# Optimization experiments

Measured on AMD Instinct MI355X. Metric: run time of the kernel, lower is better.

## Reference

```python
import jax, jax.numpy as jnp
import numpy as np

EPS = 1e-8
LN_EPS = 1e-5

def _layernorm(x, g, b):
    mu = jnp.mean(x, axis=-1, keepdims=True)
    var = jnp.mean((x - mu) ** 2, axis=-1, keepdims=True)
    return (x - mu) / jnp.sqrt(var + LN_EPS) * g + b

def setup_inputs() -> dict:
    key = jax.random.key(0)
    ks = jax.random.split(key, 10)
    B, S = 8192, 4096
    input_dim, hidden_dim = 4, 256
    h4 = hidden_dim // 4  # 64
    price_series = jax.random.uniform(ks[0], (B, S, 1), dtype=jnp.float32) + 0.5
    # 4 parallel encoders stacked on leading axis: Linear(input_dim->h4) + LayerNorm(h4)
    enc_w = jax.random.normal(ks[1], (4, input_dim, h4), dtype=jnp.float32) * 0.5
    enc_b = jax.random.normal(ks[2], (4, h4), dtype=jnp.float32) * 0.02
    enc_g = jnp.ones((4, h4), dtype=jnp.float32)
    enc_beta = jnp.zeros((4, h4), dtype=jnp.float32)
    # regime head: Linear(hidden_dim->64) + ReLU + (Dropout eval=identity) + Linear(64->4)
    head_w1 = jax.random.normal(ks[3], (hidden_dim, 64), dtype=jnp.float32) * 0.0625
    head_b1 = jnp.zeros((64,), dtype=jnp.float32)
    head_w2 = jax.random.normal(ks[4], (64, 4), dtype=jnp.float32) * 0.125
    head_b2 = jnp.zeros((4,), dtype=jnp.float32)
    return {"price_series": price_series, "enc_w": enc_w, "enc_b": enc_b,
            "enc_g": enc_g, "enc_beta": enc_beta,
            "head_w1": head_w1, "head_b1": head_b1,
            "head_w2": head_w2, "head_b2": head_b2}

def reference(price_series, enc_w, enc_b, enc_g, enc_beta, head_w1, head_b1, head_w2, head_b2):
    prices = price_series[:, :, 0]  # [B, S]
    B, S = prices.shape
    # Rolling SMA(20) with clamped window start, via cumsum (single pass, no per-step loop)
    csum = jnp.concatenate([jnp.zeros((B, 1), prices.dtype), jnp.cumsum(prices, axis=1)], axis=1)  # [B, S+1]
    i = jnp.arange(S)
    start20 = jnp.maximum(0, i - 19)
    cnt20 = (i - start20 + 1).astype(prices.dtype)
    sma20 = (csum[:, i + 1] - csum[:, start20]) / cnt20  # [B, S]
    trend_signal = (prices - sma20) / (sma20 + EPS)
    f_trend = jnp.mean(trend_signal, axis=1, keepdims=True)  # [B,1]
    # momentum over last 10 steps
    p_last = prices[:, -1:]
    p_m10 = prices[:, -10:-9]
    f_mom = (p_last - p_m10) / (p_m10 + EPS)  # [B,1]
    # mean reversion
    p_mean = jnp.mean(prices, axis=1, keepdims=True)
    f_mr = (p_last - p_mean) / (p_mean + EPS)  # [B,1]
    # cycle: coefficient of variation (torch.std is unbiased, ddof=1)
    f_cyc = jnp.std(prices, axis=1, ddof=1, keepdims=True) / (p_mean + EPS)  # [B,1]
    combined = jnp.concatenate([f_trend, f_mom, f_mr, f_cyc], axis=1)  # [B, 4]
    # 4 parallel encoders: Linear -> ReLU -> LayerNorm
    pre = jnp.einsum('bi,eio->ebo', combined, enc_w) + enc_b[:, None, :]  # [4, B, 64]
    feats = _layernorm(jax.nn.relu(pre), enc_g[:, None, :], enc_beta[:, None, :])  # [4, B, 64]
    # concat order: trend, momentum, mean_rev, cycle along feature dim
    regime_features = jnp.transpose(feats, (1, 0, 2)).reshape(B, -1)  # [B, 256]
    h = jax.nn.relu(regime_features @ head_w1 + head_b1)
    regime_probs = jax.nn.softmax(h @ head_w2 + head_b2, axis=1)  # [B, 4]
    return (regime_features, regime_probs)
```

## Files before the change

kernel.cpp:

```cpp
#include <hip/hip_runtime.h>

#define EPS 1e-8f
#define LN_EPS 1e-5f
#define NROWS 8192
#define SLEN 4096
#define PROBS_OFF 2097152
#define RPB 16

typedef __attribute__((ext_vector_type(8))) short bf16x8;
typedef __attribute__((ext_vector_type(4))) float f32x4;

__device__ __forceinline__ short f2bf(float f) {
    unsigned u = __float_as_uint(f);
    unsigned r = (u + 0x7FFFu + ((u >> 16) & 1u)) >> 16;
    return (short)r;
}

__device__ __forceinline__ void g2l16(const float4* g, float4* l) {
    __builtin_amdgcn_global_load_lds(
        (const __attribute__((address_space(1))) unsigned int*)g,
        (__attribute__((address_space(3))) unsigned int*)l,
        16, 0, 0);
}

__device__ __forceinline__ int swz(int s) { return s ^ ((s >> 3) & 7); }

__global__ __launch_bounds__(256) void k_fused(
    const float* __restrict__ prices, float* __restrict__ out,
    const float* __restrict__ enc_w, const float* __restrict__ enc_b,
    const float* __restrict__ enc_g, const float* __restrict__ enc_bt,
    const float* __restrict__ w1, const float* __restrict__ b1,
    const float* __restrict__ w2, const float* __restrict__ b2)
{
    __shared__ float4 sbuf[3][1032];
    __shared__ float red[4][3];
    __shared__ __align__(16) float comb[RPB][4];
    __shared__ short rfb[RPB][264];
    __shared__ float hbuf[RPB][68];

    const int t = threadIdx.x;
    const int lane = t & 63, wv = t >> 6;
    const int r0 = blockIdx.x * RPB;

    auto stage = [&](int r, int bi) {
        const float4* R4 = (const float4*)prices + (size_t)(r0 + r) * 1024;
        #pragma unroll
        for (int k = 0; k < 4; ++k) {
            const int base = 8 + 256 * k + 64 * wv;
            const int g = swz(base + lane) - 8;
            g2l16(R4 + g, &sbuf[bi][base]);
        }
    };

    float pm10_l = 0.f, plast_l = 0.f;

    auto compute_row = [&](int bi) {
        float4 q0 = sbuf[bi][swz(4 * t + 3)];
        float4 q1 = sbuf[bi][swz(4 * t + 4)];
        float4 q2 = sbuf[bi][swz(4 * t + 5)];
        float4 q3 = sbuf[bi][swz(4 * t + 6)];
        float4 q4 = sbuf[bi][swz(4 * t + 7)];
        float4 s0 = sbuf[bi][swz(4 * t + 8)];
        float4 s1 = sbuf[bi][swz(4 * t + 9)];
        float4 s2 = sbuf[bi][swz(4 * t + 10)];
        float4 s3 = sbuf[bi][swz(4 * t + 11)];

        float xv[16] = { s0.x, s0.y, s0.z, s0.w, s1.x, s1.y, s1.z, s1.w,
                         s2.x, s2.y, s2.z, s2.w, s3.x, s3.y, s3.z, s3.w };
        float ov[16] = { q0.x, q0.y, q0.z, q0.w, q1.x, q1.y, q1.z, q1.w,
                         q2.x, q2.y, q2.z, q2.w, q3.x, q3.y, q3.z, q3.w };

        float W = q0.y + q0.z + q0.w
                + q1.x + q1.y + q1.z + q1.w
                + q2.x + q2.y + q2.z + q2.w
                + q3.x + q3.y + q3.z + q3.w
                + q4.x + q4.y + q4.z + q4.w;

        float sum = 0.0f, sq = 0.0f, ts = 0.0f;
        if (t >= 2) {
            #pragma unroll
            for (int j = 0; j < 16; ++j) {
                float x = xv[j];
                W += (j == 0) ? x : (x - ov[j]);
                sum += x;
                sq = fmaf(x, x, sq);
                float num = fmaf(x, 20.0f, -W);
                float den = W + (20.0f * EPS);
                ts += num * __builtin_amdgcn_rcpf(den);
            }
        } else {
            const float pf = (float)(16 * t);
            #pragma unroll
            for (int j = 0; j < 16; ++j) {
                float x = xv[j];
                W += (j == 0) ? x : (x - ov[j]);
                sum += x;
                sq = fmaf(x, x, sq);
                float c = fminf(pf + (float)(j + 1), 20.0f);
                float num = fmaf(x, c, -W);
                float den = fmaf(EPS, c, W);
                ts += num * __builtin_amdgcn_rcpf(den);
            }
        }
        if (t == 255) { pm10_l = s1.z; plast_l = s3.w; }

        #pragma unroll
        for (int off = 32; off > 0; off >>= 1) {
            sum += __shfl_xor(sum, off);
            sq  += __shfl_xor(sq,  off);
            ts  += __shfl_xor(ts,  off);
        }
        if (lane == 0) { red[wv][0] = sum; red[wv][1] = sq; red[wv][2] = ts; }
    };

    auto finish_row = [&](int r) {
        if (t == 255) {
            float S = red[0][0] + red[1][0] + red[2][0] + red[3][0];
            float Q = red[0][1] + red[1][1] + red[2][1] + red[3][1];
            float T = red[0][2] + red[1][2] + red[2][2] + red[3][2];
            float mean = S * (1.0f / 4096.0f);
            float var  = fmaxf((Q - 4096.0f * mean * mean) * (1.0f / 4095.0f), 0.0f);
            comb[r][0] = T * (1.0f / 4096.0f);
            comb[r][1] = (plast_l - pm10_l) / (pm10_l + EPS);
            comb[r][2] = (plast_l - mean) / (mean + EPS);
            comb[r][3] = sqrtf(var) / (mean + EPS);
        }
    };

    if (t < 8) {
        const float4 z4 = make_float4(0.f, 0.f, 0.f, 0.f);
        sbuf[0][t] = z4; sbuf[1][t] = z4; sbuf[2][t] = z4;
    }
    stage(0, 0);
    stage(1, 1);

    for (int r = 0; r < RPB - 2; ++r) {
        stage(r + 2, (r + 2) % 3);
        asm volatile("s_waitcnt vmcnt(8) lgkmcnt(0)\ns_barrier" ::: "memory");
        __builtin_amdgcn_sched_barrier(0);
        compute_row(r % 3);
        asm volatile("s_waitcnt lgkmcnt(0)\ns_barrier" ::: "memory");
        finish_row(r);
    }
    asm volatile("s_waitcnt vmcnt(4) lgkmcnt(0)\ns_barrier" ::: "memory");
    __builtin_amdgcn_sched_barrier(0);
    compute_row((RPB - 2) % 3);
    asm volatile("s_waitcnt lgkmcnt(0)\ns_barrier" ::: "memory");
    finish_row(RPB - 2);
    asm volatile("s_waitcnt vmcnt(0) lgkmcnt(0)\ns_barrier" ::: "memory");
    __builtin_amdgcn_sched_barrier(0);
    compute_row((RPB - 1) % 3);
    asm volatile("s_waitcnt lgkmcnt(0)\ns_barrier" ::: "memory");
    finish_row(RPB - 1);

    const int l15 = lane & 15, q = lane >> 4;
    const int wave = wv;

    bf16x8 bfrag[8];
    #pragma unroll
    for (int kt = 0; kt < 8; ++kt) {
        #pragma unroll
        for (int j = 0; j < 8; ++j) {
            int k = kt * 32 + q * 8 + j;
            bfrag[kt][j] = f2bf(w1[k * 64 + wave * 16 + l15]);
        }
    }
    const float ew0  = enc_w[wave * 256 + lane];
    const float ew1v = enc_w[wave * 256 + 64 + lane];
    const float ew2v = enc_w[wave * 256 + 128 + lane];
    const float ew3v = enc_w[wave * 256 + 192 + lane];
    const float ebv = enc_b[t], egv = enc_g[t], btv = enc_bt[t];

    __syncthreads();

    for (int r = 0; r < RPB; r += 2) {
        float4 cba = *(const float4*)comb[r];
        float4 cbb = *(const float4*)comb[r + 1];
        float va = fmaf(cba.x, ew0, fmaf(cba.y, ew1v, fmaf(cba.z, ew2v, fmaf(cba.w, ew3v, ebv))));
        float vb = fmaf(cbb.x, ew0, fmaf(cbb.y, ew1v, fmaf(cbb.z, ew2v, fmaf(cbb.w, ew3v, ebv))));
        va = fmaxf(va, 0.0f);
        vb = fmaxf(vb, 0.0f);
        float sma = va, smb = vb;
        #pragma unroll
        for (int off = 32; off > 0; off >>= 1) {
            sma += __shfl_xor(sma, off);
            smb += __shfl_xor(smb, off);
        }
        float mua = sma * (1.0f / 64.0f);
        float mub = smb * (1.0f / 64.0f);
        float da = va - mua, db = vb - mub;
        float vsa = da * da, vsb = db * db;
        #pragma unroll
        for (int off = 32; off > 0; off >>= 1) {
            vsa += __shfl_xor(vsa, off);
            vsb += __shfl_xor(vsb, off);
        }
        float ya = fmaf(da * rsqrtf(vsa * (1.0f / 64.0f) + LN_EPS), egv, btv);
        float yb = fmaf(db * rsqrtf(vsb * (1.0f / 64.0f) + LN_EPS), egv, btv);
        out[(size_t)(r0 + r) * 256 + t] = ya;
        out[(size_t)(r0 + r + 1) * 256 + t] = yb;
        rfb[r][t] = f2bf(ya);
        rfb[r + 1][t] = f2bf(yb);
    }
    __syncthreads();

    f32x4 acc0 = {0.f, 0.f, 0.f, 0.f};
    #pragma unroll
    for (int kt = 0; kt < 8; ++kt) {
        bf16x8 a0 = *(const bf16x8*)&rfb[l15][kt * 32 + q * 8];
        acc0 = __builtin_amdgcn_mfma_f32_16x16x32_bf16(a0, bfrag[kt], acc0, 0, 0, 0);
    }

    const int col = wave * 16 + l15;
    const float b1v = b1[col];
    #pragma unroll
    for (int rg = 0; rg < 4; ++rg)
        hbuf[q * 4 + rg][col] = fmaxf(acc0[rg] + b1v, 0.0f);
    __syncthreads();

    if (t < 4 * RPB) {
        int r = t >> 2, c = t & 3;
        float a0 = 0.f, a1 = 0.f, a2 = 0.f, a3 = 0.f;
        #pragma unroll
        for (int j = 0; j < 16; ++j) {
            a0 = fmaf(hbuf[r][j],      w2[j * 4 + c],        a0);
            a1 = fmaf(hbuf[r][16 + j], w2[(16 + j) * 4 + c], a1);
            a2 = fmaf(hbuf[r][32 + j], w2[(32 + j) * 4 + c], a2);
            a3 = fmaf(hbuf[r][48 + j], w2[(48 + j) * 4 + c], a3);
        }
        float lg = b2[c] + ((a0 + a1) + (a2 + a3));
        float mx = fmaxf(lg, __shfl_xor(lg, 1, 4));
        mx = fmaxf(mx, __shfl_xor(mx, 2, 4));
        float ex = __expf(lg - mx);
        float s2 = ex + __shfl_xor(ex, 1, 4);
        s2 += __shfl_xor(s2, 2, 4);
        out[PROBS_OFF + (size_t)(r0 + r) * 4 + c] = ex / s2;
    }
}

extern "C" void kernel_launch(void* const* d_in, const int* in_sizes, int n_in,
                              void* d_out, int out_size, void* d_ws, size_t ws_size,
                              hipStream_t stream) {
    const float* prices  = (const float*)d_in[0];
    const float* enc_w   = (const float*)d_in[1];
    const float* enc_b   = (const float*)d_in[2];
    const float* enc_g   = (const float*)d_in[3];
    const float* enc_bt  = (const float*)d_in[4];
    const float* head_w1 = (const float*)d_in[5];
    const float* head_b1 = (const float*)d_in[6];
    const float* head_w2 = (const float*)d_in[7];
    const float* head_b2 = (const float*)d_in[8];
    float* out = (float*)d_out;
    (void)d_ws; (void)ws_size;

    k_fused<<<NROWS / RPB, 256, 0, stream>>>(prices, out, enc_w, enc_b, enc_g,
                                             enc_bt, head_w1, head_b1, head_w2,
                                             head_b2);
}
```

Measured before the change: 214.5 us.

## Give each wave its own rows to drop block barriers from the streaming phase

Each wave now streams its own 4 rows in quarter-row chunks, using a per-wave 4-slot LDS ring and carrying halo values from the previous chunk. This replaces the block-wide scheme where all four waves shared one row and synchronised with s_barrier twice per row through a cross-wave LDS reduction. Statistics are reduced with wave shuffles only, and per-row features are written directly by one lane. The trade-off is a more complex halo and index path per chunk, plus per-wave waitcnt pipelining that relies on careful vmcnt accounting.

```diff
diff --git a/kernel.cpp b/kernel.cpp
--- a/kernel.cpp
+++ b/kernel.cpp
@@ -32,8 +32,8 @@
     const float* __restrict__ w1, const float* __restrict__ b1,
     const float* __restrict__ w2, const float* __restrict__ b2)
 {
-    __shared__ float4 sbuf[3][1032];
-    __shared__ float red[4][3];
+    __shared__ float4 sbuf[4][4][256];
+    __shared__ float4 zh[4][8];
     __shared__ __align__(16) float comb[RPB][4];
     __shared__ short rfb[RPB][264];
     __shared__ float hbuf[RPB][68];
@@ -42,118 +42,105 @@
     const int lane = t & 63, wv = t >> 6;
     const int r0 = blockIdx.x * RPB;
 
-    auto stage = [&](int r, int bi) {
-        const float4* R4 = (const float4*)prices + (size_t)(r0 + r) * 1024;
-        #pragma unroll
-        for (int k = 0; k < 4; ++k) {
-            const int base = 8 + 256 * k + 64 * wv;
-            const int g = swz(base + lane) - 8;
-            g2l16(R4 + g, &sbuf[bi][base]);
-        }
+    if (lane < 8) zh[wv][lane] = make_float4(0.f, 0.f, 0.f, 0.f);
+    asm volatile("s_waitcnt lgkmcnt(0)" ::: "memory");
+
+    const float4* rowbase = (const float4*)prices + (size_t)(r0 + 4 * wv) * 1024;
+
+    auto stage = [&](int g) {
+        const float4* src = rowbase + (size_t)(g >> 2) * 1024 + (g & 3) * 256;
+        float4* dst = &sbuf[wv][g & 3][0];
+        #pragma unroll
+        for (int k = 0; k < 4; ++k)
+            g2l16(src + swz(64 * k + lane), dst + 64 * k);
     };
 
-    float pm10_l = 0.f, plast_l = 0.f;
-
-    auto compute_row = [&](int bi) {
-        float4 q0 = sbuf[bi][swz(4 * t + 3)];
-        float4 q1 = sbuf[bi][swz(4 * t + 4)];
-        float4 q2 = sbuf[bi][swz(4 * t + 5)];
-        float4 q3 = sbuf[bi][swz(4 * t + 6)];
-        float4 q4 = sbuf[bi][swz(4 * t + 7)];
-        float4 s0 = sbuf[bi][swz(4 * t + 8)];
-        float4 s1 = sbuf[bi][swz(4 * t + 9)];
-        float4 s2 = sbuf[bi][swz(4 * t + 10)];
-        float4 s3 = sbuf[bi][swz(4 * t + 11)];
+    stage(0); stage(1); stage(2);
+
+    float S = 0.f, Q = 0.f, T = 0.f;
+
+    #pragma unroll
+    for (int g = 0; g < 16; ++g) {
+        const int h = g & 3;
+        if (g <= 13)      asm volatile("s_waitcnt vmcnt(8)" ::: "memory");
+        else if (g == 14) asm volatile("s_waitcnt vmcnt(4)" ::: "memory");
+        else              asm volatile("s_waitcnt vmcnt(0)" ::: "memory");
+        __builtin_amdgcn_sched_barrier(0);
+
+        const float4* cur = &sbuf[wv][h][0];
+        const float4* prv = &sbuf[wv][(g + 3) & 3][0];
+
+        float4 hq0, hq1, hq2, hq3, hq4;
+        {
+            const bool zrow = (h == 0);
+            #pragma unroll
+            for (int i = 0; i < 5; ++i) {
+                int s = 4 * lane - 5 + i;
+                const float4* bp = (s >= 0) ? cur : (zrow ? &zh[wv][0] : prv);
+                int idx = (s >= 0) ? swz(s) : (zrow ? (s + 5) : swz(s + 256));
+                float4 v = bp[idx];
+                if (i == 0) hq0 = v; else if (i == 1) hq1 = v;
+                else if (i == 2) hq2 = v; else if (i == 3) hq3 = v; else hq4 = v;
+            }
+        }
+        float4 s0 = cur[swz(4 * lane)];
+        float4 s1 = cur[swz(4 * lane + 1)];
+        float4 s2 = cur[swz(4 * lane + 2)];
+        float4 s3 = cur[swz(4 * lane + 3)];
+
+        asm volatile("s_waitcnt lgkmcnt(0)" ::: "memory");
+        __builtin_amdgcn_sched_barrier(0);
+        if (g + 3 < 16) stage(g + 3);
 
         float xv[16] = { s0.x, s0.y, s0.z, s0.w, s1.x, s1.y, s1.z, s1.w,
                          s2.x, s2.y, s2.z, s2.w, s3.x, s3.y, s3.z, s3.w };
-        float ov[16] = { q0.x, q0.y, q0.z, q0.w, q1.x, q1.y, q1.z, q1.w,
-                         q2.x, q2.y, q2.z, q2.w, q3.x, q3.y, q3.z, q3.w };
-
-        float W = q0.y + q0.z + q0.w
-                + q1.x + q1.y + q1.z + q1.w
-                + q2.x + q2.y + q2.z + q2.w
-                + q3.x + q3.y + q3.z + q3.w
-                + q4.x + q4.y + q4.z + q4.w;
-
-        float sum = 0.0f, sq = 0.0f, ts = 0.0f;
-        if (t >= 2) {
+        float ov[16] = { hq0.x, hq0.y, hq0.z, hq0.w, hq1.x, hq1.y, hq1.z, hq1.w,
+                         hq2.x, hq2.y, hq2.z, hq2.w, hq3.x, hq3.y, hq3.z, hq3.w };
+
+        float W = hq0.y + hq0.z + hq0.w
+                + hq1.x + hq1.y + hq1.z + hq1.w
+                + hq2.x + hq2.y + hq2.z + hq2.w
+                + hq3.x + hq3.y + hq3.z + hq3.w
+                + hq4.x + hq4.y + hq4.z + hq4.w;
+
+        const float pf = (float)(1024 * h + 16 * lane);
+        #pragma unroll
+        for (int j = 0; j < 16; ++j) {
+            float x = xv[j];
+            W += (j == 0) ? x : (x - ov[j]);
+            S += x;
+            Q = fmaf(x, x, Q);
+            float c = fminf(pf + (float)(j + 1), 20.0f);
+            float num = fmaf(x, c, -W);
+            float den = fmaf(EPS, c, W);
+            T += num * __builtin_amdgcn_rcpf(den);
+        }
+
+        if (h == 3) {
+            float s_ = S, q_ = Q, t_ = T;
             #pragma unroll
-            for (int j = 0; j < 16; ++j) {
-                float x = xv[j];
-                W += (j == 0) ? x : (x - ov[j]);
-                sum += x;
-                sq = fmaf(x, x, sq);
-                float num = fmaf(x, 20.0f, -W);
-                float den = W + (20.0f * EPS);
-                ts += num * __builtin_amdgcn_rcpf(den);
+            for (int off = 32; off > 0; off >>= 1) {
+                s_ += __shfl_xor(s_, off);
+                q_ += __shfl_xor(q_, off);
+                t_ += __shfl_xor(t_, off);
             }
-        } else {
-            const float pf = (float)(16 * t);
-            #pragma unroll
-            for (int j = 0; j < 16; ++j) {
-                float x = xv[j];
-                W += (j == 0) ? x : (x - ov[j]);
-                sum += x;
-                sq = fmaf(x, x, sq);
-                float c = fminf(pf + (float)(j + 1), 20.0f);
-                float num = fmaf(x, c, -W);
-                float den = fmaf(EPS, c, W);
-                ts += num * __builtin_amdgcn_rcpf(den);
+            if (lane == 63) {
+                float mean = s_ * (1.0f / 4096.0f);
+                float var  = fmaxf((q_ - 4096.0f * mean * mean) * (1.0f / 4095.0f), 0.0f);
+                float p_m10 = xv[6];
+                float p_last = xv[15];
+                float4 f;
+                f.x = t_ * (1.0f / 4096.0f);
+                f.y = (p_last - p_m10) / (p_m10 + EPS);
+                f.z = (p_last - mean) / (mean + EPS);
+                f.w = sqrtf(var) / (mean + EPS);
+                *(float4*)comb[4 * wv + (g >> 2)] = f;
             }
-        }
-        if (t == 255) { pm10_l = s1.z; plast_l = s3.w; }
-
-        #pragma unroll
-        for (int off = 32; off > 0; off >>= 1) {
-            sum += __shfl_xor(sum, off);
-            sq  += __shfl_xor(sq,  off);
-            ts  += __shfl_xor(ts,  off);
-        }
-        if (lane == 0) { red[wv][0] = sum; red[wv][1] = sq; red[wv][2] = ts; }
-    };
-
-    auto finish_row = [&](int r) {
-        if (t == 255) {
-            float S = red[0][0] + red[1][0] + red[2][0] + red[3][0];
-            float Q = red[0][1] + red[1][1] + red[2][1] + red[3][1];
-            float T = red[0][2] + red[1][2] + red[2][2] + red[3][2];
-            float mean = S * (1.0f / 4096.0f);
-            float var  = fmaxf((Q - 4096.0f * mean * mean) * (1.0f / 4095.0f), 0.0f);
-            comb[r][0] = T * (1.0f / 4096.0f);
-            comb[r][1] = (plast_l - pm10_l) / (pm10_l + EPS);
-            comb[r][2] = (plast_l - mean) / (mean + EPS);
-            comb[r][3] = sqrtf(var) / (mean + EPS);
-        }
-    };
-
-    if (t < 8) {
-        const float4 z4 = make_float4(0.f, 0.f, 0.f, 0.f);
-        sbuf[0][t] = z4; sbuf[1][t] = z4; sbuf[2][t] = z4;
-    }
-    stage(0, 0);
-    stage(1, 1);
-
-    for (int r = 0; r < RPB - 2; ++r) {
-        stage(r + 2, (r + 2) % 3);
-        asm volatile("s_waitcnt vmcnt(8) lgkmcnt(0)\ns_barrier" ::: "memory");
-        __builtin_amdgcn_sched_barrier(0);
-        compute_row(r % 3);
-        asm volatile("s_waitcnt lgkmcnt(0)\ns_barrier" ::: "memory");
-        finish_row(r);
-    }
-    asm volatile("s_waitcnt vmcnt(4) lgkmcnt(0)\ns_barrier" ::: "memory");
-    __builtin_amdgcn_sched_barrier(0);
-    compute_row((RPB - 2) % 3);
-    asm volatile("s_waitcnt lgkmcnt(0)\ns_barrier" ::: "memory");
-    finish_row(RPB - 2);
-    asm volatile("s_waitcnt vmcnt(0) lgkmcnt(0)\ns_barrier" ::: "memory");
-    __builtin_amdgcn_sched_barrier(0);
-    compute_row((RPB - 1) % 3);
-    asm volatile("s_waitcnt lgkmcnt(0)\ns_barrier" ::: "memory");
-    finish_row(RPB - 1);
-
-    const int l15 = lane & 15, q = lane >> 4;
+            S = Q = T = 0.f;
+        }
+    }
+
+    const int l15 = lane & 15, qh = lane >> 4;
     const int wave = wv;
 
     bf16x8 bfrag[8];
@@ -161,7 +148,7 @@
     for (int kt = 0; kt < 8; ++kt) {
         #pragma unroll
         for (int j = 0; j < 8; ++j) {
-            int k = kt * 32 + q * 8 + j;
+            int k = kt * 32 + qh * 8 + j;
             bfrag[kt][j] = f2bf(w1[k * 64 + wave * 16 + l15]);
         }
     }
@@ -207,7 +194,7 @@
     f32x4 acc0 = {0.f, 0.f, 0.f, 0.f};
     #pragma unroll
     for (int kt = 0; kt < 8; ++kt) {
-        bf16x8 a0 = *(const bf16x8*)&rfb[l15][kt * 32 + q * 8];
+        bf16x8 a0 = *(const bf16x8*)&rfb[l15][kt * 32 + qh * 8];
         acc0 = __builtin_amdgcn_mfma_f32_16x16x32_bf16(a0, bfrag[kt], acc0, 0, 0, 0);
     }
 
@@ -215,7 +202,7 @@
     const float b1v = b1[col];
     #pragma unroll
     for (int rg = 0; rg < 4; ++rg)
-        hbuf[q * 4 + rg][col] = fmaxf(acc0[rg] + b1v, 0.0f);
+        hbuf[qh * 4 + rg][col] = fmaxf(acc0[rg] + b1v, 0.0f);
     __syncthreads();
 
     if (t < 4 * RPB) {
```

After: 212.9 us. Within noise of the previous version (-0.7%).
